# Optimization experiments

Hardware: AMD Instinct MI355X
Metric: run time of the kernel (lower is better)

The kernel has to match this reference:

```python
import jax, jax.numpy as jnp
import numpy as np

N_EXPERTS = 32
TOP_K = 8
N_GROUP = 4
TOPK_GROUP = 2
ROUTED_SCALING = 2.5


def setup_inputs() -> dict:
    key = jax.random.key(0)
    ks = jax.random.split(key, 9)
    B, S, H, I = 2, 512, 1024, 512
    w = 0.02
    return {
        "hidden_states": jax.random.normal(ks[0], (B, S, H), jnp.float32),
        "gate_w": jax.random.normal(ks[1], (N_EXPERTS, H), jnp.float32) * w,
        "gate_bias": jax.random.normal(ks[2], (N_EXPERTS,), jnp.float32) * w,
        "expert_gate": jax.random.normal(ks[3], (N_EXPERTS, I, H), jnp.float32) * w,
        "expert_up": jax.random.normal(ks[4], (N_EXPERTS, I, H), jnp.float32) * w,
        "expert_down": jax.random.normal(ks[5], (N_EXPERTS, H, I), jnp.float32) * w,
        "shared_gate": jax.random.normal(ks[6], (2 * I, H), jnp.float32) * w,
        "shared_up": jax.random.normal(ks[7], (2 * I, H), jnp.float32) * w,
        "shared_down": jax.random.normal(ks[8], (H, 2 * I), jnp.float32) * w,
    }


def _gate(x, gate_w, gate_bias):
    # DeepseekV3TopkRouter: sigmoid scores + bias-corrected group-limited top-k
    T, E = x.shape[0], gate_w.shape[0]
    logits = jnp.einsum("th,eh->te", x, gate_w)
    scores = jax.nn.sigmoid(logits)                       # [T,E]
    scores_choice = scores + gate_bias[None, :]
    # group score = sum of top-2 biased scores within each group
    grp = scores_choice.reshape(T, N_GROUP, E // N_GROUP)
    top2, _ = jax.lax.top_k(grp, 2)
    group_scores = top2.sum(-1)                           # [T,n_group]
    _, grp_idx = jax.lax.top_k(group_scores, TOPK_GROUP)  # [T,topk_group]
    group_mask = jax.nn.one_hot(grp_idx, N_GROUP, dtype=scores.dtype).sum(1)  # [T,n_group]
    expert_mask = jnp.repeat(group_mask, E // N_GROUP, axis=1)                # [T,E]
    masked = jnp.where(expert_mask > 0, scores_choice, 0.0)
    _, topk_idx = jax.lax.top_k(masked, TOP_K)            # [T,K]
    topk_w = jnp.take_along_axis(scores, topk_idx, axis=1)
    topk_w = topk_w / (topk_w.sum(-1, keepdims=True) + 1e-20)  # norm_topk_prob
    topk_w = topk_w * ROUTED_SCALING
    return topk_idx, topk_w


def _mlp(x, wg, wu, wd):
    return jnp.einsum("...i,hi->...h", jax.nn.silu(jnp.einsum("...h,ih->...i", x, wg)) * jnp.einsum("...h,ih->...i", x, wu), wd)


def reference(hidden_states, gate_w, gate_bias, expert_gate, expert_up, expert_down, shared_gate, shared_up, shared_down):
    orig_shape = hidden_states.shape
    H = orig_shape[-1]
    residuals = hidden_states
    x = hidden_states.reshape(-1, H)                      # [T,H]

    topk_idx, topk_w = _gate(x, gate_w, gate_bias)        # [T,K] int, [T,K] float

    # calibrate_all_experts=True: every expert processes the full token batch
    g = jnp.einsum("th,eih->eti", x, expert_gate)
    u = jnp.einsum("th,eih->eti", x, expert_up)
    outs = jnp.einsum("eti,ehi->eth", jax.nn.silu(g) * u, expert_down)  # [E,T,H]

    # combine: gather each token's top-k expert outputs, weighted sum (index_add equivalent)
    outs_t = jnp.transpose(outs, (1, 0, 2))               # [T,E,H]
    gathered = jnp.take_along_axis(outs_t, topk_idx[:, :, None], axis=1)  # [T,K,H]
    final = (gathered * topk_w[:, :, None]).sum(1)        # [T,H]

    shared = _mlp(residuals, shared_gate, shared_up, shared_down)
    return final.reshape(orig_shape) + shared
```

## Files before the change

kernel.cpp:

```cpp
#include <hip/hip_runtime.h>
#include <hip/hip_bf16.h>


typedef __attribute__((ext_vector_type(8))) short short8v;
typedef __attribute__((ext_vector_type(4))) float f32x4;

#define GLOAD_LDS(gp, lp)                                                      \
  __builtin_amdgcn_global_load_lds(                                            \
      (const __attribute__((address_space(1))) void*)(gp),                     \
      (__attribute__((address_space(3))) void*)(lp), 16, 0, 0)

__device__ __forceinline__ unsigned short f2bf(float f) {
  unsigned int u = __float_as_uint(f);
  u = (u + 0x7fffu + ((u >> 16) & 1u)) >> 16;
  return (unsigned short)u;
}
__device__ __forceinline__ float bf2f(unsigned short b) {
  return __uint_as_float(((unsigned int)b) << 16);
}

__global__ void convert_kernel(const float* __restrict__ src,
                               unsigned short* __restrict__ dst, long n) {
  long i = ((long)blockIdx.x * blockDim.x + threadIdx.x) * 4;
  long stride = (long)gridDim.x * blockDim.x * 4;
  for (; i < n; i += stride) {
    float4 v = *(const float4*)(src + i);
    ushort4 o;
    o.x = f2bf(v.x); o.y = f2bf(v.y); o.z = f2bf(v.z); o.w = f2bf(v.w);
    *(ushort4*)(dst + i) = o;
  }
}

__global__ void gate_kernel(const float* __restrict__ x, const float* __restrict__ gw,
                            const float* __restrict__ gb, float* __restrict__ W) {
  int t = blockIdx.x;
  int tid = threadIdx.x;
  __shared__ float partial[256];
  __shared__ float logits[32];
  const float* xr = x + (long)t * 1024;
  int e = tid & 31, c = tid >> 5;
  const float* wr = gw + (long)e * 1024 + c * 128;
  const float* xc = xr + c * 128;
  float s = 0.f;
  for (int h = 0; h < 128; h += 4) {
    float4 xv = *(const float4*)(xc + h);
    float4 wv = *(const float4*)(wr + h);
    s += xv.x * wv.x + xv.y * wv.y + xv.z * wv.z + xv.w * wv.w;
  }
  partial[tid] = s;
  __syncthreads();
  if (tid < 32) {
    float l = 0.f;
    for (int cc = 0; cc < 8; cc++) l += partial[tid + 32 * cc];
    logits[tid] = l;
  }
  __syncthreads();
  if (tid == 0) {
    float scores[32], sc[32];
    for (int i = 0; i < 32; i++) {
      float s1 = 1.f / (1.f + expf(-logits[i]));
      scores[i] = s1;
      sc[i] = s1 + gb[i];
    }
    float gsc[4];
    for (int g = 0; g < 4; g++) {
      float m1 = -1e30f, m2 = -1e30f;
      for (int j = 0; j < 8; j++) {
        float v = sc[g * 8 + j];
        if (v > m1) { m2 = m1; m1 = v; }
        else if (v > m2) m2 = v;
      }
      gsc[g] = m1 + m2;
    }
    int g1 = 0;
    for (int g = 1; g < 4; g++) if (gsc[g] > gsc[g1]) g1 = g;
    int g2 = -1;
    for (int g = 0; g < 4; g++) {
      if (g == g1) continue;
      if (g2 < 0 || gsc[g] > gsc[g2]) g2 = g;
    }
    float masked[32];
    for (int i = 0; i < 32; i++) {
      int g = i >> 3;
      masked[i] = (g == g1 || g == g2) ? sc[i] : 0.0f;
    }
    int idx[8]; float tw[8]; float wsum = 0.f;
    for (int k = 0; k < 8; k++) {
      int best = 0; float bv = -1e30f;
      for (int i = 0; i < 32; i++) if (masked[i] > bv) { bv = masked[i]; best = i; }
      idx[k] = best;
      masked[best] = -2e30f;
      tw[k] = scores[best];
      wsum += tw[k];
    }
    float inv = 2.5f / (wsum + 1e-20f);
    float wout[32];
    for (int i = 0; i < 32; i++) wout[i] = 0.f;
    for (int k = 0; k < 8; k++) wout[idx[k]] = tw[k] * inv;
    for (int i = 0; i < 32; i++) W[t * 32 + i] = wout[i];
  }
}

__global__ void build_lists_kernel(const float* __restrict__ W, int* __restrict__ counts,
                                   int* __restrict__ tok) {
  int i = blockIdx.x * blockDim.x + threadIdx.x;
  if (i < 32768) {
    if (W[i] != 0.f) {
      int t = i >> 5, e = i & 31;
      int p = atomicAdd(&counts[e], 1);
      tok[e * 1024 + p] = t;
    }
  }
}

__global__ void plan_kernel(const int* __restrict__ counts, int* __restrict__ plan) {
  if (threadIdx.x != 0 || blockIdx.x != 0) return;
  int n = 0, base = 0;
  for (int e = 0; e < 32; e++) {
    int c = counts[e];
    plan[224 + e] = base;
    for (int m0 = 0; m0 < c; m0 += 64) plan[1 + n++] = (e << 16) | m0;
    base += (c + 63) & ~63;
  }
  plan[0] = n;
}

__global__ void gather_rows_kernel(const unsigned short* __restrict__ xb,
                                   const int* __restrict__ counts,
                                   const int* __restrict__ tok,
                                   const int* __restrict__ plan,
                                   unsigned short* __restrict__ Xc) {
  int row = blockIdx.x * 2 + (threadIdx.x >> 7);
  int e = row >> 10, r = row & 1023;
  int cnt = counts[e];
  int pad = (cnt + 63) & ~63;
  if (r >= pad) return;
  long drow = plan[224 + e] + r;
  int c8 = (threadIdx.x & 127) * 8;
  if (r < cnt) {
    long tk = tok[e * 1024 + r];
    *(short8v*)(Xc + drow * 1024 + c8) = *(const short8v*)(xb + tk * 1024 + c8);
  } else {
    short8v z = {0, 0, 0, 0, 0, 0, 0, 0};
    *(short8v*)(Xc + drow * 1024 + c8) = z;
  }
}

__global__ __launch_bounds__(256) void gu64_kernel(
    const unsigned short* __restrict__ A, const unsigned short* __restrict__ BgAll,
    const unsigned short* __restrict__ BuAll, unsigned short* __restrict__ Act,
    const int* __restrict__ plan, const int* __restrict__ counts,
    const int* __restrict__ tok, const float* __restrict__ W,
    int K, int ldO, long strideB) {
  __shared__ unsigned short As[64 * 64];
  __shared__ unsigned short Bgs[128 * 64];
  __shared__ unsigned short Bus[128 * 64];
  int e, m0, count;
  long abase;
  if (plan) {
    if ((int)blockIdx.y >= plan[0]) return;
    int it = plan[1 + blockIdx.y];
    e = it >> 16; m0 = it & 0xffff;
    count = counts[e];
    abase = plan[224 + e];
  } else {
    e = 0; m0 = blockIdx.y * 64; count = 1 << 30; abase = 0;
  }
  int n0 = blockIdx.x * 128;
  const unsigned short* Ae = A + abase * K;
  const unsigned short* Bg = BgAll + (long)e * strideB;
  const unsigned short* Bu = BuAll + (long)e * strideB;
  unsigned short* ActE = Act + abase * ldO;

  int tid = threadIdx.x, lane = tid & 63, w = tid >> 6;
  int lrow = lane >> 3, lslot = lane & 7, csrc = lslot ^ lrow;
  int wr = w >> 1, wc = w & 1, lm = lane & 15, lk = lane >> 4;

  f32x4 zero = {0.f, 0.f, 0.f, 0.f};
  f32x4 accg[2][4], accu[2][4];
#pragma unroll
  for (int mi = 0; mi < 2; mi++)
#pragma unroll
    for (int ni = 0; ni < 4; ni++) { accg[mi][ni] = zero; accu[mi][ni] = zero; }

  for (int k0 = 0; k0 < K; k0 += 64) {
    __syncthreads();
#pragma unroll
    for (int r = 0; r < 2; r++) {
      int s = w * 2 + r;
      GLOAD_LDS(Ae + (long)(m0 + s * 8 + lrow) * K + k0 + csrc * 8, As + s * 512);
    }
#pragma unroll
    for (int r = 0; r < 4; r++) {
      int s = w * 4 + r;
      GLOAD_LDS(Bg + (long)(n0 + s * 8 + lrow) * K + k0 + csrc * 8, Bgs + s * 512);
    }
#pragma unroll
    for (int r = 0; r < 4; r++) {
      int s = w * 4 + r;
      GLOAD_LDS(Bu + (long)(n0 + s * 8 + lrow) * K + k0 + csrc * 8, Bus + s * 512);
    }
    __syncthreads();
#pragma unroll
    for (int ks = 0; ks < 2; ks++) {
      short8v af[2], bg[4], bu[4];
#pragma unroll
      for (int mi = 0; mi < 2; mi++) {
        int rA = wr * 32 + mi * 16 + lm;
        int cA = ks * 4 + lk;
        af[mi] = *(const short8v*)(As + rA * 64 + ((cA ^ (rA & 7)) * 8));
      }
#pragma unroll
      for (int ni = 0; ni < 4; ni++) {
        int rB = wc * 64 + ni * 16 + lm;
        int cB = ks * 4 + lk;
        bg[ni] = *(const short8v*)(Bgs + rB * 64 + ((cB ^ (rB & 7)) * 8));
        bu[ni] = *(const short8v*)(Bus + rB * 64 + ((cB ^ (rB & 7)) * 8));
      }
#pragma unroll
      for (int mi = 0; mi < 2; mi++)
#pragma unroll
        for (int ni = 0; ni < 4; ni++) {
          accg[mi][ni] = __builtin_amdgcn_mfma_f32_16x16x32_bf16(af[mi], bg[ni],
                                                                 accg[mi][ni], 0, 0, 0);
          accu[mi][ni] = __builtin_amdgcn_mfma_f32_16x16x32_bf16(af[mi], bu[ni],
                                                                 accu[mi][ni], 0, 0, 0);
        }
    }
  }
#pragma unroll
  for (int mi = 0; mi < 2; mi++) {
#pragma unroll
    for (int j = 0; j < 4; j++) {
      int row = m0 + wr * 32 + mi * 16 + lk * 4 + j;
      if (row >= count) continue;
      float wv = 1.f;
      if (W) wv = W[tok[(long)e * 1024 + row] * 32 + e];
#pragma unroll
      for (int ni = 0; ni < 4; ni++) {
        int col = n0 + wc * 64 + ni * 16 + lm;
        float gf = accg[mi][ni][j], uf = accu[mi][ni][j];
        ActE[(long)row * ldO + col] = f2bf(gf / (1.f + expf(-gf)) * uf * wv);
      }
    }
  }
}

__global__ __launch_bounds__(256) void down64_kernel(
    const unsigned short* __restrict__ A, const unsigned short* __restrict__ BAll,
    float* __restrict__ C, const int* __restrict__ plan, const int* __restrict__ counts,
    const int* __restrict__ tok, int K, long strideB) {
  __shared__ unsigned short As[64 * 64];
  __shared__ unsigned short Bs[128 * 64];
  int e, m0, count;
  long abase;
  if (plan) {
    if ((int)blockIdx.y >= plan[0]) return;
    int it = plan[1 + blockIdx.y];
    e = it >> 16; m0 = it & 0xffff;
    count = counts[e];
    abase = plan[224 + e];
  } else {
    e = 0; m0 = blockIdx.y * 64; count = 1 << 30; abase = 0;
  }
  int n0 = blockIdx.x * 128;
  const unsigned short* Ae = A + abase * K;
  const unsigned short* Be = BAll + (long)e * strideB;

  int tid = threadIdx.x, lane = tid & 63, w = tid >> 6;
  int lrow = lane >> 3, lslot = lane & 7, csrc = lslot ^ lrow;
  int wr = w >> 1, wc = w & 1, lm = lane & 15, lk = lane >> 4;

  f32x4 zero = {0.f, 0.f, 0.f, 0.f};
  f32x4 acc[2][4];
#pragma unroll
  for (int mi = 0; mi < 2; mi++)
#pragma unroll
    for (int ni = 0; ni < 4; ni++) acc[mi][ni] = zero;

  for (int k0 = 0; k0 < K; k0 += 64) {
    __syncthreads();
#pragma unroll
    for (int r = 0; r < 2; r++) {
      int s = w * 2 + r;
      GLOAD_LDS(Ae + (long)(m0 + s * 8 + lrow) * K + k0 + csrc * 8, As + s * 512);
    }
#pragma unroll
    for (int r = 0; r < 4; r++) {
      int s = w * 4 + r;
      GLOAD_LDS(Be + (long)(n0 + s * 8 + lrow) * K + k0 + csrc * 8, Bs + s * 512);
    }
    __syncthreads();
#pragma unroll
    for (int ks = 0; ks < 2; ks++) {
      short8v af[2], bv[4];
#pragma unroll
      for (int mi = 0; mi < 2; mi++) {
        int rA = wr * 32 + mi * 16 + lm;
        int cA = ks * 4 + lk;
        af[mi] = *(const short8v*)(As + rA * 64 + ((cA ^ (rA & 7)) * 8));
      }
#pragma unroll
      for (int ni = 0; ni < 4; ni++) {
        int rB = wc * 64 + ni * 16 + lm;
        int cB = ks * 4 + lk;
        bv[ni] = *(const short8v*)(Bs + rB * 64 + ((cB ^ (rB & 7)) * 8));
      }
#pragma unroll
      for (int mi = 0; mi < 2; mi++)
#pragma unroll
        for (int ni = 0; ni < 4; ni++)
          acc[mi][ni] = __builtin_amdgcn_mfma_f32_16x16x32_bf16(af[mi], bv[ni],
                                                                acc[mi][ni], 0, 0, 0);
    }
  }
#pragma unroll
  for (int mi = 0; mi < 2; mi++) {
#pragma unroll
    for (int j = 0; j < 4; j++) {
      int row = m0 + wr * 32 + mi * 16 + lk * 4 + j;
      if (row >= count) continue;
      long tk = tok ? tok[(long)e * 1024 + row] : row;
#pragma unroll
      for (int ni = 0; ni < 4; ni++) {
        int col = n0 + wc * 64 + ni * 16 + lm;
        atomicAdd(&C[tk * 1024 + col], acc[mi][ni][j]);
      }
    }
  }
}

extern "C" void kernel_launch(void* const* d_in, const int* in_sizes, int n_in,
                              void* d_out, int out_size, void* d_ws, size_t ws_size,
                              hipStream_t stream) {
  const float* x  = (const float*)d_in[0];
  const float* gw = (const float*)d_in[1];
  const float* gb = (const float*)d_in[2];
  const float* eg = (const float*)d_in[3];
  const float* eu = (const float*)d_in[4];
  const float* ed = (const float*)d_in[5];
  const float* sg = (const float*)d_in[6];
  const float* su = (const float*)d_in[7];
  const float* sd = (const float*)d_in[8];
  float* out = (float*)d_out;

  char* ws = (char*)d_ws;
  size_t off = 0;
  auto alloc = [&](size_t bytes) {
    off = (off + 255) & ~(size_t)255;
    void* p = ws + off;
    off += bytes;
    return p;
  };
  unsigned short* xb    = (unsigned short*)alloc(1048576L * 2);
  unsigned short* egb   = (unsigned short*)alloc(16777216L * 2);
  unsigned short* eub   = (unsigned short*)alloc(16777216L * 2);
  unsigned short* edb   = (unsigned short*)alloc(16777216L * 2);
  unsigned short* sgb   = (unsigned short*)alloc(1048576L * 2);
  unsigned short* sub   = (unsigned short*)alloc(1048576L * 2);
  unsigned short* sdb   = (unsigned short*)alloc(1048576L * 2);
  float*          Wrt   = (float*)alloc(1024L * 32 * 4);
  unsigned short* Xc    = (unsigned short*)alloc(10240L * 1024 * 2);
  unsigned short* act_c = (unsigned short*)alloc(10240L * 512 * 2);
  unsigned short* act_s = (unsigned short*)alloc(1048576L * 2);
  int*            counts = (int*)alloc(32 * 4);
  int*            tok    = (int*)alloc(32L * 1024 * 4);
  int*            plan   = (int*)alloc(256 * 4);

  hipMemsetAsync(counts, 0, 32 * 4, stream);
  hipMemsetAsync(d_out, 0, (size_t)out_size * 4, stream);

  convert_kernel<<<1024, 256, 0, stream>>>(x, xb, 1048576L);
  convert_kernel<<<4096, 256, 0, stream>>>(eg, egb, 16777216L);
  convert_kernel<<<4096, 256, 0, stream>>>(eu, eub, 16777216L);
  convert_kernel<<<4096, 256, 0, stream>>>(ed, edb, 16777216L);
  convert_kernel<<<1024, 256, 0, stream>>>(sg, sgb, 1048576L);
  convert_kernel<<<1024, 256, 0, stream>>>(su, sub, 1048576L);
  convert_kernel<<<1024, 256, 0, stream>>>(sd, sdb, 1048576L);

  gate_kernel<<<1024, 256, 0, stream>>>(x, gw, gb, Wrt);
  build_lists_kernel<<<128, 256, 0, stream>>>(Wrt, counts, tok);
  plan_kernel<<<1, 64, 0, stream>>>(counts, plan);
  gather_rows_kernel<<<16384, 256, 0, stream>>>(xb, counts, tok, plan, Xc);

  dim3 blk(256);
  gu64_kernel<<<dim3(4, 192), blk, 0, stream>>>(Xc, egb, eub, act_c, plan, counts, tok,
                                                Wrt, 1024, 512, 524288L);
  gu64_kernel<<<dim3(8, 16), blk, 0, stream>>>(xb, sgb, sub, act_s, nullptr, nullptr,
                                               nullptr, nullptr, 1024, 1024, 0L);
  down64_kernel<<<dim3(8, 192), blk, 0, stream>>>(act_c, edb, out, plan, counts, tok,
                                                  512, 524288L);
  down64_kernel<<<dim3(8, 16), blk, 0, stream>>>(act_s, sdb, out, nullptr, nullptr,
                                                 nullptr, 1024, 0L);
}
```

Measured before the change: 436.1 us.

## Merge expert and shared MLP launches into unified planned grids, batch conversions

Replaces the separate expert and shared gate/up and down launches with single kernels driven by a flattened work plan. Shared-expert tiles are placed first, and each plan entry encodes expert, m-tile and n-tile. The seven fp32-to-bf16 conversion launches are merged into two segmented kernels. The gate kernel's top-k selection is rewritten branch-free with unrolled loops and a removal bitmask. The goal is fewer launches and less launch-gap overhead, plus no idle blocks on 2D grids sized for the worst case. The cost is extra per-element segment selection in the converters and a larger plan buffer.

```diff
diff --git a/kernel.cpp b/kernel.cpp
--- a/kernel.cpp
+++ b/kernel.cpp
@@ -15,19 +15,39 @@
   u = (u + 0x7fffu + ((u >> 16) & 1u)) >> 16;
   return (unsigned short)u;
 }
-__device__ __forceinline__ float bf2f(unsigned short b) {
-  return __uint_as_float(((unsigned int)b) << 16);
-}
-
-__global__ void convert_kernel(const float* __restrict__ src,
-                               unsigned short* __restrict__ dst, long n) {
+
+__global__ void convert3_kernel(const float* __restrict__ s0, const float* __restrict__ s1,
+                                const float* __restrict__ s2, unsigned short* __restrict__ d0,
+                                unsigned short* __restrict__ d1, unsigned short* __restrict__ d2) {
   long i = ((long)blockIdx.x * blockDim.x + threadIdx.x) * 4;
   long stride = (long)gridDim.x * blockDim.x * 4;
-  for (; i < n; i += stride) {
-    float4 v = *(const float4*)(src + i);
+  for (; i < 50331648L; i += stride) {
+    int seg = (int)(i >> 24);
+    long off = i & 16777215L;
+    const float* s = seg == 0 ? s0 : (seg == 1 ? s1 : s2);
+    unsigned short* d = seg == 0 ? d0 : (seg == 1 ? d1 : d2);
+    float4 v = *(const float4*)(s + off);
     ushort4 o;
     o.x = f2bf(v.x); o.y = f2bf(v.y); o.z = f2bf(v.z); o.w = f2bf(v.w);
-    *(ushort4*)(dst + i) = o;
+    *(ushort4*)(d + off) = o;
+  }
+}
+
+__global__ void convert4_kernel(const float* __restrict__ s0, const float* __restrict__ s1,
+                                const float* __restrict__ s2, const float* __restrict__ s3,
+                                unsigned short* __restrict__ d0, unsigned short* __restrict__ d1,
+                                unsigned short* __restrict__ d2, unsigned short* __restrict__ d3) {
+  long i = ((long)blockIdx.x * blockDim.x + threadIdx.x) * 4;
+  long stride = (long)gridDim.x * blockDim.x * 4;
+  for (; i < 4194304L; i += stride) {
+    int seg = (int)(i >> 20);
+    long off = i & 1048575L;
+    const float* s = seg == 0 ? s0 : (seg == 1 ? s1 : (seg == 2 ? s2 : s3));
+    unsigned short* d = seg == 0 ? d0 : (seg == 1 ? d1 : (seg == 2 ? d2 : d3));
+    float4 v = *(const float4*)(s + off);
+    ushort4 o;
+    o.x = f2bf(v.x); o.y = f2bf(v.y); o.z = f2bf(v.z); o.w = f2bf(v.w);
+    *(ushort4*)(d + off) = o;
   }
 }
 
@@ -57,47 +77,62 @@
   __syncthreads();
   if (tid == 0) {
     float scores[32], sc[32];
+#pragma unroll
     for (int i = 0; i < 32; i++) {
       float s1 = 1.f / (1.f + expf(-logits[i]));
       scores[i] = s1;
       sc[i] = s1 + gb[i];
     }
     float gsc[4];
+#pragma unroll
     for (int g = 0; g < 4; g++) {
       float m1 = -1e30f, m2 = -1e30f;
+#pragma unroll
       for (int j = 0; j < 8; j++) {
         float v = sc[g * 8 + j];
-        if (v > m1) { m2 = m1; m1 = v; }
-        else if (v > m2) m2 = v;
+        bool gt1 = v > m1;
+        float nm2 = gt1 ? m1 : (v > m2 ? v : m2);
+        m1 = gt1 ? v : m1;
+        m2 = nm2;
       }
       gsc[g] = m1 + m2;
     }
+    float b1 = gsc[0];
     int g1 = 0;
-    for (int g = 1; g < 4; g++) if (gsc[g] > gsc[g1]) g1 = g;
+#pragma unroll
+    for (int g = 1; g < 4; g++)
+      if (gsc[g] > b1) { b1 = gsc[g]; g1 = g; }
+    float b2 = -1e30f;
     int g2 = -1;
-    for (int g = 0; g < 4; g++) {
-      if (g == g1) continue;
-      if (g2 < 0 || gsc[g] > gsc[g2]) g2 = g;
-    }
-    float masked[32];
+#pragma unroll
+    for (int g = 0; g < 4; g++)
+      if (g != g1 && gsc[g] > b2) { b2 = gsc[g]; g2 = g; }
+
+    unsigned removed = 0;
+    float tw[8]; int bi[8]; float wsum = 0.f;
+#pragma unroll
+    for (int k = 0; k < 8; k++) {
+      float bv = -1e30f, bs = 0.f;
+      int best = 0;
+#pragma unroll
+      for (int i = 0; i < 32; i++) {
+        int g = i >> 3;
+        float v = ((removed >> i) & 1u) ? -2e30f : ((g == g1 || g == g2) ? sc[i] : 0.0f);
+        if (v > bv) { bv = v; best = i; bs = scores[i]; }
+      }
+      removed |= 1u << best;
+      tw[k] = bs;
+      bi[k] = best;
+      wsum += bs;
+    }
+    float inv = 2.5f / (wsum + 1e-20f);
+#pragma unroll
     for (int i = 0; i < 32; i++) {
-      int g = i >> 3;
-      masked[i] = (g == g1 || g == g2) ? sc[i] : 0.0f;
-    }
-    int idx[8]; float tw[8]; float wsum = 0.f;
-    for (int k = 0; k < 8; k++) {
-      int best = 0; float bv = -1e30f;
-      for (int i = 0; i < 32; i++) if (masked[i] > bv) { bv = masked[i]; best = i; }
-      idx[k] = best;
-      masked[best] = -2e30f;
-      tw[k] = scores[best];
-      wsum += tw[k];
-    }
-    float inv = 2.5f / (wsum + 1e-20f);
-    float wout[32];
-    for (int i = 0; i < 32; i++) wout[i] = 0.f;
-    for (int k = 0; k < 8; k++) wout[idx[k]] = tw[k] * inv;
-    for (int i = 0; i < 32; i++) W[t * 32 + i] = wout[i];
+      float v = 0.f;
+#pragma unroll
+      for (int k = 0; k < 8; k++) v = (bi[k] == i) ? tw[k] * inv : v;
+      W[t * 32 + i] = v;
+    }
   }
 }
 
@@ -115,14 +150,24 @@
 
 __global__ void plan_kernel(const int* __restrict__ counts, int* __restrict__ plan) {
   if (threadIdx.x != 0 || blockIdx.x != 0) return;
-  int n = 0, base = 0;
+  int n_gu = 0, n_down = 0, base = 0;
+  for (int mt = 0; mt < 16; mt++)
+    for (int n0t = 0; n0t < 8; n0t++) {
+      plan[8 + n_gu++] = (32 << 8) | (mt << 4) | n0t;
+      plan[1024 + n_down++] = (32 << 8) | (mt << 4) | n0t;
+    }
   for (int e = 0; e < 32; e++) {
     int c = counts[e];
-    plan[224 + e] = base;
-    for (int m0 = 0; m0 < c; m0 += 64) plan[1 + n++] = (e << 16) | m0;
-    base += (c + 63) & ~63;
-  }
-  plan[0] = n;
+    plan[4096 + e] = base;
+    int mts = (c + 63) >> 6;
+    for (int mt = 0; mt < mts; mt++) {
+      for (int n0t = 0; n0t < 4; n0t++) plan[8 + n_gu++] = (e << 8) | (mt << 4) | n0t;
+      for (int n0t = 0; n0t < 8; n0t++) plan[1024 + n_down++] = (e << 8) | (mt << 4) | n0t;
+    }
+    base += mts * 64;
+  }
+  plan[0] = n_gu;
+  plan[1] = n_down;
 }
 
 __global__ void gather_rows_kernel(const unsigned short* __restrict__ xb,
@@ -135,7 +180,7 @@
   int cnt = counts[e];
   int pad = (cnt + 63) & ~63;
   if (r >= pad) return;
-  long drow = plan[224 + e] + r;
+  long drow = plan[4096 + e] + r;
   int c8 = (threadIdx.x & 127) * 8;
   if (r < cnt) {
     long tk = tok[e * 1024 + r];
@@ -146,31 +191,36 @@
   }
 }
 
-__global__ __launch_bounds__(256) void gu64_kernel(
-    const unsigned short* __restrict__ A, const unsigned short* __restrict__ BgAll,
-    const unsigned short* __restrict__ BuAll, unsigned short* __restrict__ Act,
+__global__ __launch_bounds__(256) void gu_all_kernel(
+    const unsigned short* __restrict__ Xc, const unsigned short* __restrict__ xb,
+    const unsigned short* __restrict__ egb, const unsigned short* __restrict__ eub,
+    const unsigned short* __restrict__ sgb, const unsigned short* __restrict__ sub,
+    unsigned short* __restrict__ act_c, unsigned short* __restrict__ act_s,
     const int* __restrict__ plan, const int* __restrict__ counts,
-    const int* __restrict__ tok, const float* __restrict__ W,
-    int K, int ldO, long strideB) {
+    const int* __restrict__ tok, const float* __restrict__ W) {
   __shared__ unsigned short As[64 * 64];
   __shared__ unsigned short Bgs[128 * 64];
   __shared__ unsigned short Bus[128 * 64];
-  int e, m0, count;
-  long abase;
-  if (plan) {
-    if ((int)blockIdx.y >= plan[0]) return;
-    int it = plan[1 + blockIdx.y];
-    e = it >> 16; m0 = it & 0xffff;
+  int id = blockIdx.x;
+  if (id >= plan[0]) return;
+  int it = plan[8 + id];
+  int e = it >> 8, mt = (it >> 4) & 15, n0 = (it & 15) * 128;
+  int m0 = mt * 64;
+  bool expert = e < 32;
+  const unsigned short *Ae, *Bg, *Bu;
+  unsigned short* Act;
+  int count, ldO;
+  if (expert) {
+    int abase = plan[4096 + e];
+    Ae = Xc + (long)abase * 1024;
+    Bg = egb + (long)e * 524288;
+    Bu = eub + (long)e * 524288;
+    Act = act_c + (long)abase * 512;
+    ldO = 512;
     count = counts[e];
-    abase = plan[224 + e];
   } else {
-    e = 0; m0 = blockIdx.y * 64; count = 1 << 30; abase = 0;
-  }
-  int n0 = blockIdx.x * 128;
-  const unsigned short* Ae = A + abase * K;
-  const unsigned short* Bg = BgAll + (long)e * strideB;
-  const unsigned short* Bu = BuAll + (long)e * strideB;
-  unsigned short* ActE = Act + abase * ldO;
+    Ae = xb; Bg = sgb; Bu = sub; Act = act_s; ldO = 1024; count = 1024;
+  }
 
   int tid = threadIdx.x, lane = tid & 63, w = tid >> 6;
   int lrow = lane >> 3, lslot = lane & 7, csrc = lslot ^ lrow;
@@ -183,22 +233,22 @@
 #pragma unroll
     for (int ni = 0; ni < 4; ni++) { accg[mi][ni] = zero; accu[mi][ni] = zero; }
 
-  for (int k0 = 0; k0 < K; k0 += 64) {
+  for (int k0 = 0; k0 < 1024; k0 += 64) {
     __syncthreads();
 #pragma unroll
     for (int r = 0; r < 2; r++) {
       int s = w * 2 + r;
-      GLOAD_LDS(Ae + (long)(m0 + s * 8 + lrow) * K + k0 + csrc * 8, As + s * 512);
+      GLOAD_LDS(Ae + (long)(m0 + s * 8 + lrow) * 1024 + k0 + csrc * 8, As + s * 512);
     }
 #pragma unroll
     for (int r = 0; r < 4; r++) {
       int s = w * 4 + r;
-      GLOAD_LDS(Bg + (long)(n0 + s * 8 + lrow) * K + k0 + csrc * 8, Bgs + s * 512);
+      GLOAD_LDS(Bg + (long)(n0 + s * 8 + lrow) * 1024 + k0 + csrc * 8, Bgs + s * 512);
     }
 #pragma unroll
     for (int r = 0; r < 4; r++) {
       int s = w * 4 + r;
-      GLOAD_LDS(Bu + (long)(n0 + s * 8 + lrow) * K + k0 + csrc * 8, Bus + s * 512);
+      GLOAD_LDS(Bu + (long)(n0 + s * 8 + lrow) * 1024 + k0 + csrc * 8, Bus + s * 512);
     }
     __syncthreads();
 #pragma unroll
@@ -234,38 +284,41 @@
     for (int j = 0; j < 4; j++) {
       int row = m0 + wr * 32 + mi * 16 + lk * 4 + j;
       if (row >= count) continue;
-      float wv = 1.f;
-      if (W) wv = W[tok[(long)e * 1024 + row] * 32 + e];
+      float wv = expert ? W[tok[(long)e * 1024 + row] * 32 + e] : 1.f;
 #pragma unroll
       for (int ni = 0; ni < 4; ni++) {
         int col = n0 + wc * 64 + ni * 16 + lm;
         float gf = accg[mi][ni][j], uf = accu[mi][ni][j];
-        ActE[(long)row * ldO + col] = f2bf(gf / (1.f + expf(-gf)) * uf * wv);
-      }
-    }
-  }
-}
-
-__global__ __launch_bounds__(256) void down64_kernel(
-    const unsigned short* __restrict__ A, const unsigned short* __restrict__ BAll,
+        Act[(long)row * ldO + col] = f2bf(gf / (1.f + expf(-gf)) * uf * wv);
+      }
+    }
+  }
+}
+
+__global__ __launch_bounds__(256) void down_all_kernel(
+    const unsigned short* __restrict__ act_c, const unsigned short* __restrict__ act_s,
+    const unsigned short* __restrict__ edb, const unsigned short* __restrict__ sdb,
     float* __restrict__ C, const int* __restrict__ plan, const int* __restrict__ counts,
-    const int* __restrict__ tok, int K, long strideB) {
+    const int* __restrict__ tok) {
   __shared__ unsigned short As[64 * 64];
   __shared__ unsigned short Bs[128 * 64];
-  int e, m0, count;
-  long abase;
-  if (plan) {
-    if ((int)blockIdx.y >= plan[0]) return;
-    int it = plan[1 + blockIdx.y];
-    e = it >> 16; m0 = it & 0xffff;
+  int id = blockIdx.x;
+  if (id >= plan[1]) return;
+  int it = plan[1024 + id];
+  int e = it >> 8, mt = (it >> 4) & 15, n0 = (it & 15) * 128;
+  int m0 = mt * 64;
+  bool expert = e < 32;
+  const unsigned short *Ae, *Be;
+  int count, K;
+  if (expert) {
+    int abase = plan[4096 + e];
+    Ae = act_c + (long)abase * 512;
+    Be = edb + (long)e * 524288;
+    K = 512;
     count = counts[e];
-    abase = plan[224 + e];
   } else {
-    e = 0; m0 = blockIdx.y * 64; count = 1 << 30; abase = 0;
-  }
-  int n0 = blockIdx.x * 128;
-  const unsigned short* Ae = A + abase * K;
-  const unsigned short* Be = BAll + (long)e * strideB;
+    Ae = act_s; Be = sdb; K = 1024; count = 1024;
+  }
 
   int tid = threadIdx.x, lane = tid & 63, w = tid >> 6;
   int lrow = lane >> 3, lslot = lane & 7, csrc = lslot ^ lrow;
@@ -320,7 +373,7 @@
     for (int j = 0; j < 4; j++) {
       int row = m0 + wr * 32 + mi * 16 + lk * 4 + j;
       if (row >= count) continue;
-      long tk = tok ? tok[(long)e * 1024 + row] : row;
+      long tk = expert ? tok[(long)e * 1024 + row] : row;
 #pragma unroll
       for (int ni = 0; ni < 4; ni++) {
         int col = n0 + wc * 64 + ni * 16 + lm;
@@ -365,31 +418,21 @@
   unsigned short* act_s = (unsigned short*)alloc(1048576L * 2);
   int*            counts = (int*)alloc(32 * 4);
   int*            tok    = (int*)alloc(32L * 1024 * 4);
-  int*            plan   = (int*)alloc(256 * 4);
+  int*            plan   = (int*)alloc(8192 * 4);
 
   hipMemsetAsync(counts, 0, 32 * 4, stream);
   hipMemsetAsync(d_out, 0, (size_t)out_size * 4, stream);
 
-  convert_kernel<<<1024, 256, 0, stream>>>(x, xb, 1048576L);
-  convert_kernel<<<4096, 256, 0, stream>>>(eg, egb, 16777216L);
-  convert_kernel<<<4096, 256, 0, stream>>>(eu, eub, 16777216L);
-  convert_kernel<<<4096, 256, 0, stream>>>(ed, edb, 16777216L);
-  convert_kernel<<<1024, 256, 0, stream>>>(sg, sgb, 1048576L);
-  convert_kernel<<<1024, 256, 0, stream>>>(su, sub, 1048576L);
-  convert_kernel<<<1024, 256, 0, stream>>>(sd, sdb, 1048576L);
+  convert3_kernel<<<4096, 256, 0, stream>>>(eg, eu, ed, egb, eub, edb);
+  convert4_kernel<<<1024, 256, 0, stream>>>(x, sg, su, sd, xb, sgb, sub, sdb);
 
   gate_kernel<<<1024, 256, 0, stream>>>(x, gw, gb, Wrt);
   build_lists_kernel<<<128, 256, 0, stream>>>(Wrt, counts, tok);
   plan_kernel<<<1, 64, 0, stream>>>(counts, plan);
   gather_rows_kernel<<<16384, 256, 0, stream>>>(xb, counts, tok, plan, Xc);
 
-  dim3 blk(256);
-  gu64_kernel<<<dim3(4, 192), blk, 0, stream>>>(Xc, egb, eub, act_c, plan, counts, tok,
-                                                Wrt, 1024, 512, 524288L);
-  gu64_kernel<<<dim3(8, 16), blk, 0, stream>>>(xb, sgb, sub, act_s, nullptr, nullptr,
-                                               nullptr, nullptr, 1024, 1024, 0L);
-  down64_kernel<<<dim3(8, 192), blk, 0, stream>>>(act_c, edb, out, plan, counts, tok,
-                                                  512, 524288L);
-  down64_kernel<<<dim3(8, 16), blk, 0, stream>>>(act_s, sdb, out, nullptr, nullptr,
-                                                 nullptr, 1024, 0L);
-}
+  gu_all_kernel<<<768, 256, 0, stream>>>(Xc, xb, egb, eub, sgb, sub, act_c, act_s,
+                                         plan, counts, tok, Wrt);
+  down_all_kernel<<<1408, 256, 0, stream>>>(act_c, act_s, edb, sdb, out, plan, counts,
+                                            tok);
+}
```

New measurement: 411.7 us. -5.6%, faster.
